# Optimization experiments

Hardware: AMD Instinct MI355X
Metric: run time of the kernel (lower is better)

Reference implementation:

```python
import jax, jax.numpy as jnp
import numpy as np

D_MODEL = 768
D_STATE = 16
D_CONV = 4
EXPAND = 2
N_LAYERS = 8
VOCAB = 512
MAXSEQ = 2048
BATCH = 8
SEQ = 2048
D_INNER = EXPAND * D_MODEL
N_EMO, N_STY, N_KEY, N_MODE = 8, 8, 12, 2


def setup_inputs() -> dict:
    key = jax.random.key(0)
    ks = jax.random.split(key, 32)
    def nrm(k, shape, s=0.02):
        return (jax.random.normal(k, shape) * s).astype(jnp.float32)
    inp = {}
    inp['tokens'] = jax.random.randint(ks[0], (BATCH, SEQ), 0, VOCAB)
    inp['emotion'] = jax.random.randint(ks[1], (BATCH,), 0, N_EMO)
    inp['style'] = jax.random.randint(ks[2], (BATCH,), 0, N_STY)
    inp['key_sig'] = jax.random.randint(ks[3], (BATCH,), 0, N_KEY)
    inp['mode'] = jax.random.randint(ks[4], (BATCH,), 0, N_MODE)
    inp['bpm'] = (jax.random.uniform(ks[5], (BATCH,)) * 140.0 + 60.0).astype(jnp.float32)
    inp['tok_emb'] = nrm(ks[6], (VOCAB, D_MODEL))
    inp['emo_emb'] = nrm(ks[7], (N_EMO, D_MODEL))
    inp['sty_emb'] = nrm(ks[8], (N_STY, D_MODEL))
    inp['key_emb'] = nrm(ks[9], (N_KEY, D_MODEL))
    inp['mode_emb'] = nrm(ks[10], (N_MODE, D_MODEL))
    inp['bpm_w'] = nrm(ks[11], (D_MODEL, 1))
    inp['bpm_b'] = jnp.zeros((D_MODEL,), jnp.float32)
    inp['cond_w'] = nrm(ks[12], (D_MODEL, 5 * D_MODEL))
    inp['cond_b'] = jnp.zeros((D_MODEL,), jnp.float32)
    inp['pos_emb'] = nrm(ks[13], (MAXSEQ, D_MODEL))
    inp['ln_g'] = jnp.ones((N_LAYERS, D_MODEL), jnp.float32)
    inp['ln_b'] = jnp.zeros((N_LAYERS, D_MODEL), jnp.float32)
    inp['in_w'] = nrm(ks[14], (N_LAYERS, 2 * D_INNER, D_MODEL))
    inp['conv_w'] = nrm(ks[15], (N_LAYERS, D_INNER, 1, D_CONV), 0.1)
    inp['xproj_w'] = nrm(ks[16], (N_LAYERS, 2 * D_STATE, D_INNER))
    inp['dt_w'] = nrm(ks[17], (N_LAYERS, D_INNER, D_STATE))
    inp['dt_b'] = jnp.zeros((N_LAYERS, D_INNER), jnp.float32)
    inp['bproj_w'] = nrm(ks[18], (N_LAYERS, D_INNER, D_STATE))
    inp['d_param'] = jnp.ones((N_LAYERS, D_INNER), jnp.float32)
    inp['out_w'] = nrm(ks[19], (N_LAYERS, D_MODEL, D_INNER))
    inp['final_g'] = jnp.ones((D_MODEL,), jnp.float32)
    inp['final_b'] = jnp.zeros((D_MODEL,), jnp.float32)
    inp['head_w'] = nrm(ks[20], (VOCAB, D_MODEL))
    inp['head_b'] = jnp.zeros((VOCAB,), jnp.float32)
    return inp


def _layernorm(x, g, b):
    mu = x.mean(-1, keepdims=True)
    v = ((x - mu) ** 2).mean(-1, keepdims=True)
    return (x - mu) * jax.lax.rsqrt(v + 1e-5) * g + b


def _silu(x):
    return x * jax.nn.sigmoid(x)


def _mamba_block(x, in_w, conv_w, xproj_w, dt_w, dt_b, bproj_w, d_param, out_w):
    B, L, _ = x.shape
    xz = x @ in_w.T                       # [B,L,2*di]
    xc, z = jnp.split(xz, 2, axis=-1)
    # causal depthwise conv1d: torch pads d_conv-1 both sides then slices [:L]
    xt = jnp.transpose(xc, (0, 2, 1))     # [B,di,L]
    xt = jax.lax.conv_general_dilated(xt, conv_w, (1,), [(D_CONV - 1, 0)],
                                      feature_group_count=D_INNER)
    xc = _silu(jnp.transpose(xt, (0, 2, 1)))   # [B,L,di]
    dt_raw, b_raw = jnp.split(xc @ xproj_w.T, 2, axis=-1)  # each [B,L,ds]
    delta = jnp.clip(jax.nn.softplus(dt_raw @ dt_w.T + dt_b), 1e-4, 1.0)  # [B,L,di]
    bp = b_raw @ bproj_w.T                 # [B,L,di]

    def step(h, inputs):
        d, u, bb = inputs
        h = h * (1.0 - d) + u * bb
        return h, h

    xs = (jnp.transpose(delta, (1, 0, 2)),
          jnp.transpose(xc, (1, 0, 2)),
          jnp.transpose(bp, (1, 0, 2)))    # time-major [L,B,di]
    h0 = jnp.zeros((B, D_INNER), x.dtype)
    _, ys = jax.lax.scan(step, h0, xs)
    y = jnp.transpose(ys, (1, 0, 2)) + d_param * xc
    y = y * _silu(z)
    return y @ out_w.T


def reference(tokens, emotion, style, key_sig, mode, bpm, tok_emb, emo_emb, sty_emb,
              key_emb, mode_emb, bpm_w, bpm_b, cond_w, cond_b, pos_emb, ln_g, ln_b,
              in_w, conv_w, xproj_w, dt_w, dt_b, bproj_w, d_param, out_w,
              final_g, final_b, head_w, head_b):
    B, L = tokens.shape
    cond = jnp.concatenate([
        emo_emb[emotion], sty_emb[style], key_emb[key_sig], mode_emb[mode],
        bpm[:, None] @ bpm_w.T + bpm_b], axis=-1)       # [B,5d]
    cond = cond @ cond_w.T + cond_b                      # [B,d]
    x = tok_emb[tokens] + cond[:, None, :] + pos_emb[:L][None]
    for i in range(N_LAYERS):
        res = x
        h = _layernorm(x, ln_g[i], ln_b[i])
        x = res + _mamba_block(h, in_w[i], conv_w[i], xproj_w[i], dt_w[i],
                               dt_b[i], bproj_w[i], d_param[i], out_w[i])
    x = _layernorm(x, final_g, final_b)
    return x @ head_w.T + head_b
```

## Files before the change

### kernel.cpp

```cpp
#include <hip/hip_runtime.h>
#include <cstdint>

#define BATCH 8
#define SEQ   2048
#define DM    768
#define DI    1536
#define DS    16
#define NL    8
#define NVOCAB 512
#define BT    (BATCH*SEQ)
#define NCHUNK 32
#define TC    (SEQ/NCHUNK)

typedef __attribute__((ext_vector_type(8))) short bf16x8;
typedef __attribute__((ext_vector_type(4))) float f32x4;

__device__ __forceinline__ unsigned short f2bf(float f){
  unsigned int u = __float_as_uint(f);
  u += 0x7fffu + ((u >> 16) & 1u);
  return (unsigned short)(u >> 16);
}
__device__ __forceinline__ float bf2f(unsigned short s){
  return __uint_as_float(((unsigned int)s) << 16);
}
__device__ __forceinline__ float sigm(float x){ return 1.0f/(1.0f + __expf(-x)); }
__device__ __forceinline__ float siluf(float x){ return x * sigm(x); }
__device__ __forceinline__ float fast_softplus(float x){
  return (x > 15.0f) ? x : __logf(1.0f + __expf(x));
}
__device__ __forceinline__ void async16(void* l, const void* g){
  __builtin_amdgcn_global_load_lds(
      (const __attribute__((address_space(1))) unsigned int*)g,
      (__attribute__((address_space(3))) unsigned int*)l, 16, 0, 0);
}
__device__ __forceinline__ float dot4(f32x4 a, f32x4 b){
  return fmaf(a[0],b[0], fmaf(a[1],b[1], fmaf(a[2],b[2], a[3]*b[3])));
}

__global__ void cvt_bf16_kernel(const float4* __restrict__ in, ushort4* __restrict__ out, int n4){
  int i = blockIdx.x*256 + threadIdx.x;
  int stride = gridDim.x*256;
  for(; i<n4; i+=stride){
    float4 v = in[i];
    ushort4 o; o.x=f2bf(v.x); o.y=f2bf(v.y); o.z=f2bf(v.z); o.w=f2bf(v.w);
    out[i]=o;
  }
}

__global__ void wcomb_kernel(const float* __restrict__ dt_w, const float* __restrict__ bproj_w,
                             unsigned short* __restrict__ out){
  int idx = blockIdx.x*256 + threadIdx.x;
  int k = idx & 31, ld = idx >> 5;
  float v = (k < 16) ? dt_w[(long)ld*16 + k] : bproj_w[(long)ld*16 + (k-16)];
  out[idx] = f2bf(v);
}

__global__ __launch_bounds__(256) void cond_kernel(const int* __restrict__ emotion,
    const int* __restrict__ style, const int* __restrict__ keysig, const int* __restrict__ modei,
    const float* __restrict__ bpm, const float* __restrict__ emo_emb, const float* __restrict__ sty_emb,
    const float* __restrict__ key_emb, const float* __restrict__ mode_emb,
    const float* __restrict__ bpm_w, const float* __restrict__ bpm_b,
    const float* __restrict__ cond_w, const float* __restrict__ cond_b,
    float* __restrict__ cond_out){
  int b = blockIdx.y;
  int tid = threadIdx.x;
  __shared__ float vec[5*DM];
  int e = emotion[b], st = style[b], ks = keysig[b], md = modei[b];
  float bp = bpm[b];
  for(int j=tid; j<960; j+=256){
    int seg = j/192, o4 = j - seg*192;
    float4 v;
    if(seg==0)      v = reinterpret_cast<const float4*>(emo_emb + (long)e*DM)[o4];
    else if(seg==1) v = reinterpret_cast<const float4*>(sty_emb + (long)st*DM)[o4];
    else if(seg==2) v = reinterpret_cast<const float4*>(key_emb + (long)ks*DM)[o4];
    else if(seg==3) v = reinterpret_cast<const float4*>(mode_emb + (long)md*DM)[o4];
    else {
      float4 w = reinterpret_cast<const float4*>(bpm_w)[o4];
      float4 bb = reinterpret_cast<const float4*>(bpm_b)[o4];
      v = make_float4(fmaf(bp,w.x,bb.x), fmaf(bp,w.y,bb.y), fmaf(bp,w.z,bb.z), fmaf(bp,w.w,bb.w));
    }
    reinterpret_cast<float4*>(vec)[j] = v;
  }
  __syncthreads();
  int wid = tid>>6, lane = tid&63;
  int dm = blockIdx.x*4 + wid;
  const float4* w4 = reinterpret_cast<const float4*>(cond_w + (long)dm*(5*DM));
  const float4* v4 = reinterpret_cast<const float4*>(vec);
  float acc = 0.f;
  #pragma unroll 5
  for(int j=lane; j<960; j+=64){
    float4 w = w4[j], v = v4[j];
    acc = fmaf(w.x,v.x, fmaf(w.y,v.y, fmaf(w.z,v.z, fmaf(w.w,v.w, acc))));
  }
  #pragma unroll
  for(int off=32; off>0; off>>=1) acc += __shfl_xor(acc, off);
  if(lane==0) cond_out[b*DM + dm] = acc + cond_b[dm];
}

__global__ void embed_kernel(const int* __restrict__ tokens, const float* __restrict__ tok_emb,
    const float* __restrict__ cond, const float* __restrict__ pos_emb, float* __restrict__ x){
  int bt = blockIdx.x;
  int b = bt >> 11, t = bt & 2047;
  int tok = tokens[bt];
  const float4* te = reinterpret_cast<const float4*>(tok_emb + (long)tok*DM);
  const float4* ce = reinterpret_cast<const float4*>(cond + (long)b*DM);
  const float4* pe = reinterpret_cast<const float4*>(pos_emb + (long)t*DM);
  float4* xo = reinterpret_cast<float4*>(x + (long)bt*DM);
  int i = threadIdx.x;
  float4 a = te[i], c = ce[i], p = pe[i];
  xo[i] = make_float4(a.x+c.x+p.x, a.y+c.y+p.y, a.z+c.z+p.z, a.w+c.w+p.w);
}

__global__ __launch_bounds__(256) void ln_bf16_kernel(const float* __restrict__ x,
                     const float* __restrict__ g, const float* __restrict__ bta,
                     unsigned short* __restrict__ out){
  int row  = blockIdx.x*4 + (threadIdx.x >> 6);
  int lane = threadIdx.x & 63;
  const float* xr = x + (long)row*DM;
  float4 v[3];
  float sum=0.f, sq=0.f;
  #pragma unroll
  for(int i=0;i<3;i++){
    v[i] = *reinterpret_cast<const float4*>(xr + i*256 + lane*4);
    sum += v[i].x + v[i].y + v[i].z + v[i].w;
    sq  += v[i].x*v[i].x + v[i].y*v[i].y + v[i].z*v[i].z + v[i].w*v[i].w;
  }
  #pragma unroll
  for(int off=32; off>0; off>>=1){
    sum += __shfl_xor(sum, off);
    sq  += __shfl_xor(sq , off);
  }
  float mu  = sum * (1.0f/DM);
  float var = sq  * (1.0f/DM) - mu*mu;
  float rs  = rsqrtf(var + 1e-5f);
  unsigned short* orow = out + (long)row*DM;
  #pragma unroll
  for(int i=0;i<3;i++){
    int d = i*256 + lane*4;
    float4 gg = *reinterpret_cast<const float4*>(g + d);
    float4 bb = *reinterpret_cast<const float4*>(bta + d);
    ushort4 o;
    o.x = f2bf((v[i].x - mu)*rs*gg.x + bb.x);
    o.y = f2bf((v[i].y - mu)*rs*gg.y + bb.y);
    o.z = f2bf((v[i].z - mu)*rs*gg.z + bb.z);
    o.w = f2bf((v[i].w - mu)*rs*gg.w + bb.w);
    *reinterpret_cast<ushort4*>(orow + d) = o;
  }
}

template<int MODE>
__global__ __launch_bounds__(256) void gemm_lds(const unsigned short* __restrict__ A,
                                               const unsigned short* __restrict__ B,
                                               void* __restrict__ Cv,
                                               const float* __restrict__ bias,
                                               int K, int ldc){
  __shared__ short As[128*64];
  __shared__ short Bs[128*64];
  const short* Ap = (const short*)A;
  const short* Bp = (const short*)B;
  int tid  = threadIdx.x;
  int lane = tid & 63;
  int wid  = tid >> 6;

  int nbx = gridDim.x;
  int id  = blockIdx.y*nbx + blockIdx.x;
  int q   = (nbx*gridDim.y) >> 3;
  int swz = (id & 7)*q + (id >> 3);
  int bx  = swz % nbx, by = swz / nbx;
  int row0 = by*128;
  int col0 = bx*128;

  int srow[4], goff[4];
  #pragma unroll
  for(int j=0;j<4;j++){
    int c = j*256 + tid;
    int row = c>>3, s = c&7;
    srow[j] = row;
    goff[j] = (s ^ (row&7))*8;
  }

  int wr = (wid>>1)*64;
  int wc = (wid&1)*64;
  int fr = lane & 15;
  int kq = lane >> 4;
  int fx = fr & 7;

  f32x4 acc[4][4];
  #pragma unroll
  for(int m=0;m<4;m++)
    #pragma unroll
    for(int n=0;n<4;n++)
      acc[m][n] = (f32x4){0.f,0.f,0.f,0.f};

  for(int kt=0; kt<K; kt+=64){
    #pragma unroll
    for(int j=0;j<4;j++){
      int c = j*256 + tid;
      async16((char*)As + c*16, Ap + (long)(row0+srow[j])*K + kt + goff[j]);
      async16((char*)Bs + c*16, Bp + (long)(col0+srow[j])*K + kt + goff[j]);
    }
    __syncthreads();
    #pragma unroll
    for(int ks=0; ks<2; ks++){
      int sA = ((ks*4 + kq) ^ fx) * 8;
      bf16x8 av[4], bv[4];
      #pragma unroll
      for(int m=0;m<4;m++)
        av[m] = *reinterpret_cast<const bf16x8*>(As + (wr + m*16 + fr)*64 + sA);
      #pragma unroll
      for(int n=0;n<4;n++)
        bv[n] = *reinterpret_cast<const bf16x8*>(Bs + (wc + n*16 + fr)*64 + sA);
      #pragma unroll
      for(int m=0;m<4;m++)
        #pragma unroll
        for(int n=0;n<4;n++)
          acc[m][n] = __builtin_amdgcn_mfma_f32_16x16x32_bf16(av[m], bv[n], acc[m][n], 0, 0, 0);
    }
    __syncthreads();
  }

  int rr = (lane >> 4) << 2;
  int cc = lane & 15;
  #pragma unroll
  for(int m=0;m<4;m++){
    #pragma unroll
    for(int n=0;n<4;n++){
      int col = col0 + wc + n*16 + cc;
      #pragma unroll
      for(int i=0;i<4;i++){
        long idx = (long)(row0 + wr + m*16 + rr + i)*ldc + col;
        float v = acc[m][n][i];
        if(MODE==3)      ((unsigned short*)Cv)[idx] = f2bf(v);
        else if(MODE==1) ((float*)Cv)[idx] += v;
        else if(MODE==2) ((float*)Cv)[idx] = v + bias[col];
        else             ((float*)Cv)[idx] = v;
      }
    }
  }
}

__global__ __launch_bounds__(256) void xproj_kernel(const unsigned short* __restrict__ xz,
      const float* __restrict__ cw, const unsigned short* __restrict__ wbf,
      float* __restrict__ dtb){
  __shared__ unsigned short xcs[16][DI+8];
  __shared__ float pdt[4][16][32];
  int blk = blockIdx.x;
  int b  = blk >> 7;
  int t0 = (blk & 127) << 4;
  int tid = threadIdx.x;
  long base = ((long)b*SEQ + t0)*(2*DI);
  if(tid < 192){
    int d0 = tid*8;
    float cc0[8], cc1[8], cc2[8], cc3[8];
    #pragma unroll
    for(int j=0;j<8;j++){
      cc0[j]=cw[(d0+j)*4+0]; cc1[j]=cw[(d0+j)*4+1];
      cc2[j]=cw[(d0+j)*4+2]; cc3[j]=cw[(d0+j)*4+3];
    }
    float wm3[8], wm2[8], wm1[8];
    #pragma unroll
    for(int j=0;j<8;j++){ wm3[j]=0.f; wm2[j]=0.f; wm1[j]=0.f; }
    if(t0>0){
      bf16x8 v3 = *reinterpret_cast<const bf16x8*>(xz + base - 3*(2*DI) + d0);
      bf16x8 v2 = *reinterpret_cast<const bf16x8*>(xz + base - 2*(2*DI) + d0);
      bf16x8 v1 = *reinterpret_cast<const bf16x8*>(xz + base - 1*(2*DI) + d0);
      #pragma unroll
      for(int j=0;j<8;j++){
        wm3[j]=bf2f((unsigned short)v3[j]);
        wm2[j]=bf2f((unsigned short)v2[j]);
        wm1[j]=bf2f((unsigned short)v1[j]);
      }
    }
    for(int tt=0; tt<16; tt++){
      bf16x8 vt = *reinterpret_cast<const bf16x8*>(xz + base + (long)tt*(2*DI) + d0);
      bf16x8 o;
      #pragma unroll
      for(int j=0;j<8;j++){
        float wt = bf2f((unsigned short)vt[j]);
        float u  = cc0[j]*wm3[j] + cc1[j]*wm2[j] + cc2[j]*wm1[j] + cc3[j]*wt;
        o[j] = (short)f2bf(siluf(u));
        wm3[j]=wm2[j]; wm2[j]=wm1[j]; wm1[j]=wt;
      }
      *reinterpret_cast<bf16x8*>(&xcs[tt][d0]) = o;
    }
  }
  __syncthreads();
  int wid = tid >> 6, lane = tid & 63;
  int fr = lane & 15, kq = lane >> 4;
  f32x4 a0 = (f32x4){0.f,0.f,0.f,0.f};
  f32x4 a1 = (f32x4){0.f,0.f,0.f,0.f};
  const unsigned short* w0 = wbf + (long)fr*DI;
  const unsigned short* w1 = wbf + (long)(16+fr)*DI;
  int kbase = wid*384 + kq*8;
  #pragma unroll
  for(int ks=0; ks<12; ks++){
    int k = kbase + ks*32;
    bf16x8 av = *reinterpret_cast<const bf16x8*>(&xcs[fr][k]);
    bf16x8 b0 = *reinterpret_cast<const bf16x8*>(w0 + k);
    bf16x8 b1 = *reinterpret_cast<const bf16x8*>(w1 + k);
    a0 = __builtin_amdgcn_mfma_f32_16x16x32_bf16(av, b0, a0, 0, 0, 0);
    a1 = __builtin_amdgcn_mfma_f32_16x16x32_bf16(av, b1, a1, 0, 0, 0);
  }
  int rr = kq << 2;
  #pragma unroll
  for(int i=0;i<4;i++){
    pdt[wid][rr+i][fr]      = a0[i];
    pdt[wid][rr+i][16+fr]   = a1[i];
  }
  __syncthreads();
  for(int e = tid; e < 512; e += 256){
    int r = e >> 5, s = e & 31;
    float v = pdt[0][r][s] + pdt[1][r][s] + pdt[2][r][s] + pdt[3][r][s];
    dtb[((long)b*SEQ + t0 + r)*32 + s] = v;
  }
}

__global__ __launch_bounds__(256) void scanAY_mfma_kernel(const unsigned short* __restrict__ xz,
      const float* __restrict__ dtb, const float* __restrict__ cw,
      const unsigned short* __restrict__ wcomb,
      const float* __restrict__ dtbias_g, const float* __restrict__ dp_g,
      float2* __restrict__ chunk, unsigned short* __restrict__ y0s,
      unsigned short* __restrict__ as_s){
  __shared__ unsigned short abuf[64][32];
  __shared__ unsigned short dab[64*256*2];
  int c = blockIdx.x, db = blockIdx.y, b = blockIdx.z;
  int tid = threadIdx.x;
  int t0 = c*TC;
  {
    const float4* src = reinterpret_cast<const float4*>(dtb + ((long)b*SEQ + t0)*32);
    float4 v0 = src[tid*2], v1 = src[tid*2+1];
    bf16x8 o;
    o[0]=(short)f2bf(v0.x); o[1]=(short)f2bf(v0.y); o[2]=(short)f2bf(v0.z); o[3]=(short)f2bf(v0.w);
    o[4]=(short)f2bf(v1.x); o[5]=(short)f2bf(v1.y); o[6]=(short)f2bf(v1.z); o[7]=(short)f2bf(v1.w);
    *reinterpret_cast<bf16x8*>(&abuf[tid>>2][(tid&3)*8]) = o;
  }
  __syncthreads();
  {
    int w = tid >> 6, lane = tid & 63;
    int fr = lane & 15, kq = lane >> 4;
    bf16x8 zero = {0,0,0,0,0,0,0,0};
    bf16x8 bq[4], bp[4];
    #pragma unroll
    for(int nt=0; nt<4; nt++){
      int dcol = db*256 + w*64 + nt*16 + fr;
      bf16x8 wv = *reinterpret_cast<const bf16x8*>(wcomb + (long)dcol*32 + kq*8);
      bq[nt] = (kq<2) ? wv : zero;
      bp[nt] = (kq<2) ? zero : wv;
    }
    #pragma unroll
    for(int mt=0; mt<4; mt++){
      bf16x8 av = *reinterpret_cast<const bf16x8*>(&abuf[mt*16 + fr][kq*8]);
      #pragma unroll
      for(int nt=0; nt<4; nt++){
        f32x4 aq = __builtin_amdgcn_mfma_f32_16x16x32_bf16(av, bq[nt], (f32x4){0.f,0.f,0.f,0.f}, 0,0,0);
        f32x4 ap = __builtin_amdgcn_mfma_f32_16x16x32_bf16(av, bp[nt], (f32x4){0.f,0.f,0.f,0.f}, 0,0,0);
        int dl = w*64 + nt*16 + fr;
        #pragma unroll
        for(int i=0;i<4;i++){
          int t = mt*16 + kq*4 + i;
          unsigned int pack = (unsigned int)f2bf(aq[i]) | (((unsigned int)f2bf(ap[i]))<<16);
          *reinterpret_cast<unsigned int*>(&dab[(t*256 + dl)*2]) = pack;
        }
      }
    }
  }
  int d = db*256 + tid;
  float c0=cw[d*4],c1=cw[d*4+1],c2=cw[d*4+2],c3=cw[d*4+3];
  float bias = dtbias_g[d];
  float dp = dp_g[d];
  asm volatile("" : "+v"(c0),"+v"(c1),"+v"(c2),"+v"(c3),"+v"(bias),"+v"(dp));
  long base = ((long)b*SEQ + t0)*(2*DI) + d;
  float wm3 = (t0>0) ? bf2f(xz[base - 3*(2*DI)]) : 0.f;
  float wm2 = (t0>0) ? bf2f(xz[base - 2*(2*DI)]) : 0.f;
  float wm1 = (t0>0) ? bf2f(xz[base - 1*(2*DI)]) : 0.f;
  const unsigned short* xp = xz + base;
  long sidx = ((long)b*SEQ + t0)*DI + d;
  unsigned short* yp = y0s + sidx;
  unsigned short* ap2 = as_s + sidx;
  __syncthreads();
  float h = 0.f, P = 1.f;
  const unsigned int* dab32 = reinterpret_cast<const unsigned int*>(dab);
  for(int g=0; g<TC/8; g++){
    unsigned short xv[8];
    #pragma unroll
    for(int j=0;j<8;j++){ xv[j] = xp[(long)j*2*DI]; }
    xp += 8L*2*DI;
    #pragma unroll
    for(int j=0;j<8;j++){
      float wt = bf2f(xv[j]);
      float u = siluf(fmaf(c3,wt, fmaf(c2,wm1, fmaf(c1,wm2, c0*wm3))));
      wm3=wm2; wm2=wm1; wm1=wt;
      unsigned int pk = dab32[(g*8+j)*256 + tid];
      float da = bias + bf2f((unsigned short)(pk & 0xffffu));
      float ba = bf2f((unsigned short)(pk >> 16));
      float delta = fminf(fmaxf(fast_softplus(da), 1e-4f), 1.0f);
      float a = 1.0f - delta;
      h = fmaf(h, a, u*ba);
      P *= a;
      yp[(long)j*DI]  = f2bf(fmaf(dp, u, h));
      ap2[(long)j*DI] = f2bf(P);
    }
    yp += 8L*DI; ap2 += 8L*DI;
  }
  chunk[((long)b*DI + d)*NCHUNK + c] = make_float2(P, h);
}

__global__ __launch_bounds__(256) void scanAY_kernel(const unsigned short* __restrict__ xz,
      const float* __restrict__ dtb, const float* __restrict__ cw,
      const float* __restrict__ dtw_g, const float* __restrict__ dtbias_g,
      const float* __restrict__ bpw_g, const float* __restrict__ dp_g,
      float2* __restrict__ chunk, unsigned short* __restrict__ y,
      unsigned short* __restrict__ asz_s){
  __shared__ float dsb[TC*32];
  int c = blockIdx.x, db = blockIdx.y, b = blockIdx.z;
  int d = db*256 + threadIdx.x;
  int t0 = c*TC;
  {
    const float4* src = reinterpret_cast<const float4*>(dtb + ((long)b*SEQ + t0)*32);
    float4* dst = reinterpret_cast<float4*>(dsb);
    dst[threadIdx.x]       = src[threadIdx.x];
    dst[threadIdx.x + 256] = src[threadIdx.x + 256];
  }
  float c0=cw[d*4],c1=cw[d*4+1],c2=cw[d*4+2],c3=cw[d*4+3];
  f32x4 wq0 = *reinterpret_cast<const f32x4*>(dtw_g + d*16 + 0);
  f32x4 wq1 = *reinterpret_cast<const f32x4*>(dtw_g + d*16 + 4);
  f32x4 wq2 = *reinterpret_cast<const f32x4*>(dtw_g + d*16 + 8);
  f32x4 wq3 = *reinterpret_cast<const f32x4*>(dtw_g + d*16 + 12);
  f32x4 wp0 = *reinterpret_cast<const f32x4*>(bpw_g + d*16 + 0);
  f32x4 wp1 = *reinterpret_cast<const f32x4*>(bpw_g + d*16 + 4);
  f32x4 wp2 = *reinterpret_cast<const f32x4*>(bpw_g + d*16 + 8);
  f32x4 wp3 = *reinterpret_cast<const f32x4*>(bpw_g + d*16 + 12);
  float bias = dtbias_g[d];
  float dp = dp_g[d];
  asm volatile("" : "+v"(wq0),"+v"(wq1),"+v"(wq2),"+v"(wq3),
                    "+v"(wp0),"+v"(wp1),"+v"(wp2),"+v"(wp3),
                    "+v"(c0),"+v"(c1),"+v"(c2),"+v"(c3),"+v"(bias),"+v"(dp));
  long base = ((long)b*SEQ + t0)*(2*DI) + d;
  float wm3 = (t0>0) ? bf2f(xz[base - 3*(2*DI)]) : 0.f;
  float wm2 = (t0>0) ? bf2f(xz[base - 2*(2*DI)]) : 0.f;
  float wm1 = (t0>0) ? bf2f(xz[base - 1*(2*DI)]) : 0.f;
  const unsigned short* xp = xz + base;
  const unsigned short* zp = xz + base + DI;
  long sidx = ((long)b*SEQ + t0)*DI + d;
  unsigned short* yp = y + sidx;
  unsigned short* ap = asz_s + sidx;
  __syncthreads();
  float h = 0.f, P = 1.f;
  for(int g=0; g<TC/8; g++){
    unsigned short xv[8], zv[8];
    #pragma unroll
    for(int j=0;j<8;j++){ xv[j] = xp[(long)j*2*DI]; zv[j] = zp[(long)j*2*DI]; }
    xp += 8L*2*DI; zp += 8L*2*DI;
    const float* rp = dsb + g*8*32;
    #pragma unroll
    for(int j=0;j<8;j++){
      float wt = bf2f(xv[j]);
      float u = siluf(fmaf(c3,wt, fmaf(c2,wm1, fmaf(c1,wm2, c0*wm3))));
      wm3=wm2; wm2=wm1; wm1=wt;
      const f32x4* row = reinterpret_cast<const f32x4*>(rp + j*32);
      float da = bias + dot4(row[0],wq0) + dot4(row[1],wq1) + dot4(row[2],wq2) + dot4(row[3],wq3);
      float ba =        dot4(row[4],wp0) + dot4(row[5],wp1) + dot4(row[6],wp2) + dot4(row[7],wp3);
      float delta = fminf(fmaxf(fast_softplus(da), 1e-4f), 1.0f);
      float a = 1.0f - delta;
      h = fmaf(h, a, u*ba);
      P *= a;
      float sz = siluf(bf2f(zv[j]));
      yp[(long)j*DI] = f2bf(fmaf(dp, u, h) * sz);
      ap[(long)j*DI] = f2bf(P * sz);
    }
    yp += 8L*DI; ap += 8L*DI;
  }
  chunk[((long)b*DI + d)*NCHUNK + c] = make_float2(P, h);
}

__global__ __launch_bounds__(256) void h0_kernel(const float2* __restrict__ chunk,
                                                 float* __restrict__ h0tab){
  int idx = blockIdx.x*256 + threadIdx.x;
  int b = idx / DI, d = idx - b*DI;
  const float2* cb = chunk + ((long)b*DI + d)*NCHUNK;
  float h0 = 0.f;
  for(int c=0; c<NCHUNK; c++){
    h0tab[((long)b*NCHUNK + c)*DI + d] = h0;
    float2 ps = cb[c];
    h0 = fmaf(ps.x, h0, ps.y);
  }
}

__global__ __launch_bounds__(256) void fixup_z_kernel(const unsigned short* __restrict__ as_s,
      const float* __restrict__ h0tab, const unsigned short* __restrict__ xz,
      unsigned short* __restrict__ y){
  int i = (blockIdx.x*256 + threadIdx.x)*8;
  int bt = i / DI;
  int d  = i - bt*DI;
  int b  = bt >> 11;
  int c  = (bt & 2047) >> 6;
  const float* hp = h0tab + ((long)b*NCHUNK + c)*DI + d;
  f32x4 h0a = *reinterpret_cast<const f32x4*>(hp);
  f32x4 h0b = *reinterpret_cast<const f32x4*>(hp + 4);
  bf16x8 yv = *reinterpret_cast<const bf16x8*>(y + i);
  bf16x8 av = *reinterpret_cast<const bf16x8*>(as_s + i);
  bf16x8 zv = *reinterpret_cast<const bf16x8*>(xz + (long)bt*(2*DI) + DI + d);
  bf16x8 o;
  #pragma unroll
  for(int j=0;j<8;j++){
    float h0 = (j<4) ? h0a[j] : h0b[j-4];
    float v = fmaf(h0, bf2f((unsigned short)av[j]), bf2f((unsigned short)yv[j]));
    o[j] = (short)f2bf(v * siluf(bf2f((unsigned short)zv[j])));
  }
  *reinterpret_cast<bf16x8*>(y + i) = o;
}

__global__ __launch_bounds__(256) void fixup_kernel(const unsigned short* __restrict__ asz_s,
      const float* __restrict__ h0tab, unsigned short* __restrict__ y){
  int i = (blockIdx.x*256 + threadIdx.x)*8;
  int bt = i / DI;
  int d  = i - bt*DI;
  int b  = bt >> 11;
  int c  = (bt & 2047) >> 6;
  const float* hp = h0tab + ((long)b*NCHUNK + c)*DI + d;
  f32x4 h0a = *reinterpret_cast<const f32x4*>(hp);
  f32x4 h0b = *reinterpret_cast<const f32x4*>(hp + 4);
  bf16x8 yv = *reinterpret_cast<const bf16x8*>(y + i);
  bf16x8 av = *reinterpret_cast<const bf16x8*>(asz_s + i);
  bf16x8 o;
  #pragma unroll
  for(int j=0;j<8;j++){
    float h0 = (j<4) ? h0a[j] : h0b[j-4];
    o[j] = (short)f2bf(fmaf(h0, bf2f((unsigned short)av[j]), bf2f((unsigned short)yv[j])));
  }
  *reinterpret_cast<bf16x8*>(y + i) = o;
}

extern "C" void kernel_launch(void* const* d_in, const int* in_sizes, int n_in,
                              void* d_out, int out_size, void* d_ws, size_t ws_size,
                              hipStream_t stream){
  const int*   tokens  = (const int*)  d_in[0];
  const int*   emotion = (const int*)  d_in[1];
  const int*   style   = (const int*)  d_in[2];
  const int*   keysig  = (const int*)  d_in[3];
  const int*   modei   = (const int*)  d_in[4];
  const float* bpm     = (const float*)d_in[5];
  const float* tok_emb = (const float*)d_in[6];
  const float* emo_emb = (const float*)d_in[7];
  const float* sty_emb = (const float*)d_in[8];
  const float* key_emb = (const float*)d_in[9];
  const float* mode_emb= (const float*)d_in[10];
  const float* bpm_w   = (const float*)d_in[11];
  const float* bpm_b   = (const float*)d_in[12];
  const float* cond_w  = (const float*)d_in[13];
  const float* cond_b  = (const float*)d_in[14];
  const float* pos_emb = (const float*)d_in[15];
  const float* ln_g    = (const float*)d_in[16];
  const float* ln_b    = (const float*)d_in[17];
  const float* in_w    = (const float*)d_in[18];
  const float* conv_w  = (const float*)d_in[19];
  const float* xproj_w = (const float*)d_in[20];
  const float* dt_w    = (const float*)d_in[21];
  const float* dt_b    = (const float*)d_in[22];
  const float* bproj_w = (const float*)d_in[23];
  const float* d_param = (const float*)d_in[24];
  const float* out_w   = (const float*)d_in[25];
  const float* final_g = (const float*)d_in[26];
  const float* final_b = (const float*)d_in[27];
  const float* head_w  = (const float*)d_in[28];
  const float* head_b  = (const float*)d_in[29];

  char* ws = (char*)d_ws;
  float*          x       = (float*)(ws + 0L);
  unsigned short* hy      = (unsigned short*)(ws + 50331648L);
  unsigned short* xz      = (unsigned short*)(ws + 100663296L);
  float*          dtbuf   = (float*)(ws + 201326592L);
  float2*         chunk   = (float2*)(ws + 203423744L);
  float*          condv   = (float*)(ws + 206569472L);
  unsigned short* inwb    = (unsigned short*)(ws + 206594048L);
  unsigned short* outwb   = (unsigned short*)(ws + 211312640L);
  unsigned short* headwb  = (unsigned short*)(ws + 213671936L);
  unsigned short* wbf_all = (unsigned short*)(ws + 214458368L);
  float*          h0tab   = (float*)(ws + 215244800L);
  unsigned short* asz_s   = (unsigned short*)(ws + 216817664L);
  unsigned short* wcombb  = (unsigned short*)(ws + 267149312L);

  const bool use_y0   = (ws_size >= 267149312UL);
  const bool use_mfma = (ws_size >= 267935744UL);

  unsigned short* h_bf = hy;
  unsigned short* y_bf = hy;
  unsigned short* xfin = hy;

  cvt_bf16_kernel<<<128,256,0,stream>>>((const float4*)head_w,(ushort4*)headwb, NVOCAB*DM/4);
  cvt_bf16_kernel<<<384,256,0,stream>>>((const float4*)xproj_w,(ushort4*)wbf_all, NL*32*DI/4);
  if(use_mfma)
    wcomb_kernel<<<NL*DI*32/256,256,0,stream>>>(dt_w, bproj_w, wcombb);
  cond_kernel<<<dim3(DM/4,8),256,0,stream>>>(emotion, style, keysig, modei, bpm, emo_emb, sty_emb,
        key_emb, mode_emb, bpm_w, bpm_b, cond_w, cond_b, condv);
  embed_kernel<<<BT,192,0,stream>>>(tokens, tok_emb, condv, pos_emb, x);

  for(int l=0; l<NL; l++){
    cvt_bf16_kernel<<<1024,256,0,stream>>>((const float4*)(in_w  + (long)l*2*DI*DM), (ushort4*)inwb,  2*DI*DM/4);
    cvt_bf16_kernel<<<512, 256,0,stream>>>((const float4*)(out_w + (long)l*DM*DI),   (ushort4*)outwb, DM*DI/4);
    ln_bf16_kernel<<<BT/4,256,0,stream>>>(x, ln_g + l*DM, ln_b + l*DM, h_bf);
    gemm_lds<3><<<dim3(2*DI/128, BT/128),256,0,stream>>>(h_bf, inwb, xz, nullptr, DM, 2*DI);
    xproj_kernel<<<BT/16,256,0,stream>>>(xz, conv_w + l*DI*4, wbf_all + (long)l*32*DI, dtbuf);
    if(use_mfma){
      scanAY_mfma_kernel<<<dim3(NCHUNK,6,BATCH),256,0,stream>>>(xz, dtbuf, conv_w + l*DI*4,
            wcombb + (long)l*DI*32, dt_b + l*DI, d_param + l*DI, chunk, y_bf, asz_s);
      h0_kernel<<<48,256,0,stream>>>(chunk, h0tab);
      fixup_z_kernel<<<BT*DI/(256*8),256,0,stream>>>(asz_s, h0tab, xz, y_bf);
    } else {
      scanAY_kernel<<<dim3(NCHUNK,6,BATCH),256,0,stream>>>(xz, dtbuf, conv_w + l*DI*4,
            dt_w + l*DI*DS, dt_b + l*DI, bproj_w + l*DI*DS, d_param + l*DI, chunk, y_bf, asz_s);
      h0_kernel<<<48,256,0,stream>>>(chunk, h0tab);
      fixup_kernel<<<BT*DI/(256*8),256,0,stream>>>(asz_s, h0tab, y_bf);
    }
    gemm_lds<1><<<dim3(DM/128, BT/128),256,0,stream>>>(y_bf, outwb, x, nullptr, DI, DM);
  }
  ln_bf16_kernel<<<BT/4,256,0,stream>>>(x, final_g, final_b, xfin);
  gemm_lds<2><<<dim3(NVOCAB/128, BT/128),256,0,stream>>>(xfin, headwb, d_out, head_b, DM, NVOCAB);
}
```

Before: 2.381 ms.

## Double-buffer LDS tiles in GEMM to overlap async loads with MFMA

The GEMM kernel now uses two LDS buffers and issues the async global-to-LDS copies for the next K tile before computing on the current one. Explicit vmcnt waits and raw barriers replace __syncthreads, and s_setprio raises wave priority around the MFMA block. This hides global-load latency behind the matrix math. The cost is double the LDS use (64KB per block), which can lower occupancy.

```diff
diff --git a/kernel.cpp b/kernel.cpp
--- a/kernel.cpp
+++ b/kernel.cpp
@@ -154,8 +154,7 @@
                                                void* __restrict__ Cv,
                                                const float* __restrict__ bias,
                                                int K, int ldc){
-  __shared__ short As[128*64];
-  __shared__ short Bs[128*64];
+  __shared__ short smem[2][2][128*64];
   const short* Ap = (const short*)A;
   const short* Bp = (const short*)B;
   int tid  = threadIdx.x;
@@ -192,14 +191,31 @@
     for(int n=0;n<4;n++)
       acc[m][n] = (f32x4){0.f,0.f,0.f,0.f};
 
-  for(int kt=0; kt<K; kt+=64){
-    #pragma unroll
-    for(int j=0;j<4;j++){
-      int c = j*256 + tid;
-      async16((char*)As + c*16, Ap + (long)(row0+srow[j])*K + kt + goff[j]);
-      async16((char*)Bs + c*16, Bp + (long)(col0+srow[j])*K + kt + goff[j]);
-    }
-    __syncthreads();
+  #define STAGE(buf, kt) { \
+    char* aB = (char*)&smem[buf][0][0]; \
+    char* bB = (char*)&smem[buf][1][0]; \
+    _Pragma("unroll") \
+    for(int j=0;j<4;j++){ \
+      int c = j*256 + tid; \
+      async16(aB + c*16, Ap + (long)(row0+srow[j])*K + (kt) + goff[j]); \
+      async16(bB + c*16, Bp + (long)(col0+srow[j])*K + (kt) + goff[j]); \
+    } }
+
+  int NT = K >> 6;
+  STAGE(0, 0)
+  for(int t=0; t<NT; ++t){
+    int cur = t & 1;
+    if(t+1 < NT){
+      STAGE(cur^1, (t+1)*64)
+      asm volatile("s_waitcnt vmcnt(8)" ::: "memory");
+    } else {
+      asm volatile("s_waitcnt vmcnt(0)" ::: "memory");
+    }
+    __builtin_amdgcn_s_barrier();
+    __builtin_amdgcn_sched_barrier(0);
+    const short* As = &smem[cur][0][0];
+    const short* Bs = &smem[cur][1][0];
+    __builtin_amdgcn_s_setprio(1);
     #pragma unroll
     for(int ks=0; ks<2; ks++){
       int sA = ((ks*4 + kq) ^ fx) * 8;
@@ -216,8 +232,11 @@
         for(int n=0;n<4;n++)
           acc[m][n] = __builtin_amdgcn_mfma_f32_16x16x32_bf16(av[m], bv[n], acc[m][n], 0, 0, 0);
     }
-    __syncthreads();
-  }
+    __builtin_amdgcn_s_setprio(0);
+    __builtin_amdgcn_sched_barrier(0);
+    __builtin_amdgcn_s_barrier();
+  }
+  #undef STAGE
 
   int rr = (lane >> 4) << 2;
   int cc = lane & 15;
```

Result: slower. 2.467 ms (+3.6%).
